# Optimization experiments

Measured on AMD Instinct MI355X. Metric: run time of the kernel, lower is better.

The kernel has to match this reference:

```python
import jax, jax.numpy as jnp
import numpy as np

NORM_EPS = 1e-12  # torch F.normalize default eps (module's self.eps is unused)


def setup_inputs() -> dict:
    key = jax.random.key(0)
    k1, k2 = jax.random.split(key)
    src_feat = jax.random.normal(k1, (4, 2048, 128), dtype=jnp.float32)
    tgt_feat = jax.random.normal(k2, (4, 2048, 128), dtype=jnp.float32)
    return {"src_feat": src_feat, "tgt_feat": tgt_feat}


def reference(src_feat, tgt_feat):
    # src_feat: [B,N,C], tgt_feat: [B,M,C]
    # Cosine similarity via normalized matmul instead of [B,N,M,C] broadcast.
    src_sq = jnp.sum(src_feat * src_feat, axis=-1)          # [B,N]
    tgt_sq = jnp.sum(tgt_feat * tgt_feat, axis=-1)          # [B,M]
    src_n = src_feat / jnp.maximum(jnp.sqrt(src_sq), NORM_EPS)[..., None]
    tgt_n = tgt_feat / jnp.maximum(jnp.sqrt(tgt_sq), NORM_EPS)[..., None]
    cosine_sim = jnp.einsum('bnc,bmc->bnm', src_n, tgt_n)   # [B,N,M]
    # Squared L2 distance via ||s||^2 + ||t||^2 - 2 s.t (clamped for numerics)
    dots = jnp.einsum('bnc,bmc->bnm', src_feat, tgt_feat)   # [B,N,M]
    dist_sq = src_sq[:, :, None] + tgt_sq[:, None, :] - 2.0 * dots
    feat_dist = jnp.sqrt(jnp.maximum(dist_sq, 0.0))
    feat_dist_normalized = 1.0 / (1.0 + feat_dist)
    # [B,N,M,2]
    return jnp.stack([cosine_sim, feat_dist_normalized], axis=-1)
```

## Files before the change

kernel.cpp:

```cpp
#include <hip/hip_runtime.h>

#define BATCH 4
#define NDIM 2048
#define MDIM 2048
#define CDIM 128

typedef short bf16x8 __attribute__((ext_vector_type(8)));
typedef float f32x4  __attribute__((ext_vector_type(4)));

__device__ __forceinline__ unsigned short f2bf(float f) {
    union { float f; unsigned int u; } v; v.f = f;
    unsigned int u = v.u;
    return (unsigned short)((u + 0x7FFFu + ((u >> 16) & 1u)) >> 16);
}

__global__ __launch_bounds__(256) void norm_kernel(
    const float* __restrict__ src, const float* __restrict__ tgt,
    float* __restrict__ ws)
{
    int gid  = blockIdx.x * 256 + threadIdx.x;
    int wid  = gid >> 6;
    int lane = gid & 63;
    int row  = (wid << 1) + (lane >> 5);
    const float* base = (row < BATCH * NDIM)
        ? (src + (size_t)row * CDIM)
        : (tgt + (size_t)(row - BATCH * NDIM) * CDIM);
    float4 v = ((const float4*)base)[lane & 31];
    float s = v.x * v.x + v.y * v.y + v.z * v.z + v.w * v.w;
    #pragma unroll
    for (int off = 16; off >= 1; off >>= 1) s += __shfl_xor(s, off, 64);
    if ((lane & 31) == 0) ws[row] = s;
}

__global__ __launch_bounds__(256, 3) void sim_mfma(
    const float* __restrict__ src, const float* __restrict__ tgt,
    const float* __restrict__ ws, float* __restrict__ out)
{
    __shared__ unsigned short As[128 * 128];
    __shared__ unsigned short Bs[64 * 128];

    const int tid = threadIdx.x;
    const int b   = blockIdx.z;
    const int i0  = blockIdx.y << 7;
    const int j0  = blockIdx.x << 6;

    const float4* s4 = (const float4*)(src + ((size_t)b * NDIM + i0) * CDIM);
    const float4* t4 = (const float4*)(tgt + ((size_t)b * MDIM + j0) * CDIM);

    #pragma unroll 4
    for (int it = 0; it < 16; ++it) {
        int idx  = tid + it * 256;
        int row  = idx >> 5;
        int c4   = idx & 31;
        float4 va = s4[idx];
        int chunk = c4 >> 1;
        int half  = c4 & 1;
        int off   = row * 128 + (((chunk ^ (row & 15)) << 3) + (half << 2));
        ushort4 ua;
        ua.x = f2bf(va.x); ua.y = f2bf(va.y); ua.z = f2bf(va.z); ua.w = f2bf(va.w);
        *(ushort4*)&As[off] = ua;
    }
    #pragma unroll 4
    for (int it = 0; it < 8; ++it) {
        int idx  = tid + it * 256;
        int row  = idx >> 5;
        int c4   = idx & 31;
        float4 vb = t4[idx];
        int chunk = c4 >> 1;
        int half  = c4 & 1;
        int off   = row * 128 + (((chunk ^ (row & 15)) << 3) + (half << 2));
        ushort4 ub;
        ub.x = f2bf(vb.x); ub.y = f2bf(vb.y); ub.z = f2bf(vb.z); ub.w = f2bf(vb.w);
        *(ushort4*)&Bs[off] = ub;
    }
    __syncthreads();

    const int wave = tid >> 6;
    const int lane = tid & 63;
    const int wm   = (wave & 1) << 6;
    const int wn   = (wave >> 1) << 5;
    const int l16  = lane & 15;
    const int q    = lane >> 4;

    const float* nrmS = ws + (size_t)b * NDIM + i0;
    const float* nrmT = ws + (size_t)BATCH * NDIM + (size_t)b * MDIM + j0;

    float sq[4][4], isq[4][4];
    #pragma unroll
    for (int i = 0; i < 4; ++i) {
        float4 s4v = *(const float4*)&nrmS[wm + (i << 4) + (q << 2)];
        sq[i][0] = s4v.x; sq[i][1] = s4v.y; sq[i][2] = s4v.z; sq[i][3] = s4v.w;
        #pragma unroll
        for (int r = 0; r < 4; ++r)
            isq[i][r] = __builtin_amdgcn_rsqf(fmaxf(sq[i][r], 1e-24f));
    }
    float tq[2], itq[2];
    #pragma unroll
    for (int jh = 0; jh < 2; ++jh) {
        tq[jh]  = nrmT[wn + (jh << 4) + l16];
        itq[jh] = __builtin_amdgcn_rsqf(fmaxf(tq[jh], 1e-24f));
    }

    float2* out2 = (float2*)out;

    #pragma unroll
    for (int jh = 0; jh < 2; ++jh) {
        f32x4 acc[4];
        #pragma unroll
        for (int i = 0; i < 4; ++i) acc[i] = (f32x4){0.f, 0.f, 0.f, 0.f};

        const int brow = wn + (jh << 4) + l16;
        #pragma unroll
        for (int k0 = 0; k0 < 4; ++k0) {
            int chunk = (k0 << 2) + q;
            int swz   = (chunk ^ l16) << 3;
            bf16x8 bv = *(const bf16x8*)&Bs[brow * 128 + swz];
            #pragma unroll
            for (int i = 0; i < 4; ++i) {
                bf16x8 a = *(const bf16x8*)&As[(wm + (i << 4) + l16) * 128 + swz];
                acc[i] = __builtin_amdgcn_mfma_f32_16x16x32_bf16(a, bv, acc[i], 0, 0, 0);
            }
        }

        const int   ncol = wn + (jh << 4) + l16;
        const float tqj  = tq[jh], itj = itq[jh];
        #pragma unroll
        for (int i = 0; i < 4; ++i) {
            #pragma unroll
            for (int r = 0; r < 4; ++r) {
                int mrow = wm + (i << 4) + (q << 2) + r;
                size_t rowbase =
                    ((size_t)b * NDIM + (size_t)(i0 + mrow)) * MDIM + j0;
                float d   = acc[i][r];
                float cs  = d * isq[i][r] * itj;
                float dsq = fmaf(-2.0f, d, sq[i][r] + tqj);
                float fd  = __builtin_amdgcn_sqrtf(fmaxf(dsq, 0.0f));
                float fdn = __builtin_amdgcn_rcpf(1.0f + fd);
                out2[rowbase + ncol] = make_float2(cs, fdn);
            }
        }
    }
}

extern "C" void kernel_launch(void* const* d_in, const int* in_sizes, int n_in,
                              void* d_out, int out_size, void* d_ws, size_t ws_size,
                              hipStream_t stream) {
    const float* src = (const float*)d_in[0];
    const float* tgt = (const float*)d_in[1];
    float* ws  = (float*)d_ws;
    float* out = (float*)d_out;

    norm_kernel<<<dim3(2048), dim3(256), 0, stream>>>(src, tgt, ws);

    dim3 grid(MDIM / 64, NDIM / 128, BATCH);
    sim_mfma<<<grid, dim3(256), 0, stream>>>(src, tgt, ws, out);
}
```

Measured before the change: 147.7 us.

## Pre-convert inputs to swizzled bf16 once and stage tiles via global_load_lds

```diff
diff --git a/kernel.cpp b/kernel.cpp
--- a/kernel.cpp
+++ b/kernel.cpp
@@ -4,6 +4,7 @@
 #define NDIM 2048
 #define MDIM 2048
 #define CDIM 128
+#define NROWS (BATCH * NDIM)
 
 typedef short bf16x8 __attribute__((ext_vector_type(8)));
 typedef float f32x4  __attribute__((ext_vector_type(4)));
@@ -14,27 +15,40 @@
     return (unsigned short)((u + 0x7FFFu + ((u >> 16) & 1u)) >> 16);
 }
 
-__global__ __launch_bounds__(256) void norm_kernel(
+__device__ __forceinline__ void gload_lds16(const void* g, void* l) {
+    __builtin_amdgcn_global_load_lds(
+        (const __attribute__((address_space(1))) void*)g,
+        (__attribute__((address_space(3))) void*)l, 16, 0, 0);
+}
+
+__global__ __launch_bounds__(256) void prep_kernel(
     const float* __restrict__ src, const float* __restrict__ tgt,
-    float* __restrict__ ws)
+    unsigned short* __restrict__ bf, float* __restrict__ nrm)
 {
-    int gid  = blockIdx.x * 256 + threadIdx.x;
-    int wid  = gid >> 6;
-    int lane = gid & 63;
-    int row  = (wid << 1) + (lane >> 5);
-    const float* base = (row < BATCH * NDIM)
+    int gid = blockIdx.x * 256 + threadIdx.x;
+    int row = gid >> 5;
+    int l32 = gid & 31;
+    const float* base = (row < NROWS)
         ? (src + (size_t)row * CDIM)
-        : (tgt + (size_t)(row - BATCH * NDIM) * CDIM);
-    float4 v = ((const float4*)base)[lane & 31];
+        : (tgt + (size_t)(row - NROWS) * CDIM);
+    float4 v = ((const float4*)base)[l32];
     float s = v.x * v.x + v.y * v.y + v.z * v.z + v.w * v.w;
     #pragma unroll
     for (int off = 16; off >= 1; off >>= 1) s += __shfl_xor(s, off, 64);
-    if ((lane & 31) == 0) ws[row] = s;
+    if (l32 == 0) nrm[row] = s;
+
+    int chunk = l32 >> 1;
+    int half  = l32 & 1;
+    unsigned short* dst = bf + (size_t)row * CDIM
+                        + (((chunk ^ (row & 15)) << 3) + (half << 2));
+    ushort4 u;
+    u.x = f2bf(v.x); u.y = f2bf(v.y); u.z = f2bf(v.z); u.w = f2bf(v.w);
+    *(ushort4*)dst = u;
 }
 
 __global__ __launch_bounds__(256, 3) void sim_mfma(
-    const float* __restrict__ src, const float* __restrict__ tgt,
-    const float* __restrict__ ws, float* __restrict__ out)
+    const unsigned short* __restrict__ bfS, const unsigned short* __restrict__ bfT,
+    const float* __restrict__ nrm, float* __restrict__ out)
 {
     __shared__ unsigned short As[128 * 128];
     __shared__ unsigned short Bs[64 * 128];
@@ -44,35 +58,18 @@
     const int i0  = blockIdx.y << 7;
     const int j0  = blockIdx.x << 6;
 
-    const float4* s4 = (const float4*)(src + ((size_t)b * NDIM + i0) * CDIM);
-    const float4* t4 = (const float4*)(tgt + ((size_t)b * MDIM + j0) * CDIM);
+    const char* gA = (const char*)(bfS + ((size_t)b * NDIM + i0) * CDIM);
+    const char* gB = (const char*)(bfT + ((size_t)b * MDIM + j0) * CDIM);
+    char* lA = (char*)As;
+    char* lB = (char*)Bs;
+    const int t16 = tid << 4;
 
-    #pragma unroll 4
-    for (int it = 0; it < 16; ++it) {
-        int idx  = tid + it * 256;
-        int row  = idx >> 5;
-        int c4   = idx & 31;
-        float4 va = s4[idx];
-        int chunk = c4 >> 1;
-        int half  = c4 & 1;
-        int off   = row * 128 + (((chunk ^ (row & 15)) << 3) + (half << 2));
-        ushort4 ua;
-        ua.x = f2bf(va.x); ua.y = f2bf(va.y); ua.z = f2bf(va.z); ua.w = f2bf(va.w);
-        *(ushort4*)&As[off] = ua;
-    }
-    #pragma unroll 4
-    for (int it = 0; it < 8; ++it) {
-        int idx  = tid + it * 256;
-        int row  = idx >> 5;
-        int c4   = idx & 31;
-        float4 vb = t4[idx];
-        int chunk = c4 >> 1;
-        int half  = c4 & 1;
-        int off   = row * 128 + (((chunk ^ (row & 15)) << 3) + (half << 2));
-        ushort4 ub;
-        ub.x = f2bf(vb.x); ub.y = f2bf(vb.y); ub.z = f2bf(vb.z); ub.w = f2bf(vb.w);
-        *(ushort4*)&Bs[off] = ub;
-    }
+    #pragma unroll
+    for (int it = 0; it < 8; ++it)
+        gload_lds16(gA + t16 + it * 4096, lA + t16 + it * 4096);
+    #pragma unroll
+    for (int it = 0; it < 4; ++it)
+        gload_lds16(gB + t16 + it * 4096, lB + t16 + it * 4096);
     __syncthreads();
 
     const int wave = tid >> 6;
@@ -82,8 +79,8 @@
     const int l16  = lane & 15;
     const int q    = lane >> 4;
 
-    const float* nrmS = ws + (size_t)b * NDIM + i0;
-    const float* nrmT = ws + (size_t)BATCH * NDIM + (size_t)b * MDIM + j0;
+    const float* nrmS = nrm + (size_t)b * NDIM + i0;
+    const float* nrmT = nrm + (size_t)NROWS + (size_t)b * MDIM + j0;
 
     float sq[4][4], isq[4][4];
     #pragma unroll
@@ -147,11 +144,14 @@
                               hipStream_t stream) {
     const float* src = (const float*)d_in[0];
     const float* tgt = (const float*)d_in[1];
-    float* ws  = (float*)d_ws;
     float* out = (float*)d_out;
 
-    norm_kernel<<<dim3(2048), dim3(256), 0, stream>>>(src, tgt, ws);
+    unsigned short* bfS = (unsigned short*)d_ws;
+    unsigned short* bfT = bfS + (size_t)NROWS * CDIM;
+    float*          nrm = (float*)(bfT + (size_t)NROWS * CDIM);
+
+    prep_kernel<<<dim3(2048), dim3(256), 0, stream>>>(src, tgt, bfS, nrm);
 
     dim3 grid(MDIM / 64, NDIM / 128, BATCH);
-    sim_mfma<<<grid, dim3(256), 0, stream>>>(src, tgt, ws, out);
+    sim_mfma<<<grid, dim3(256), 0, stream>>>(bfS, bfT, nrm, out);
 }
```

Result: faster. 144.3 us (-2.3%).
